# Performance work log

Hardware: AMD Instinct MI355X
Metric: run time of the kernel (lower is better)

## Reference

```python
import jax, jax.numpy as jnp
import numpy as np

LEVELS = 3  # num_basis = 1 + 1 + 2 + 4 = 8


def _haar_basis(x):
    """Closed-form vectorized Haar basis, x: [B, F] raw inputs.

    Replaces the original nested per-feature/per-level/per-bucket mask loops:
    at each level only one bucket k = floor(u*freq) is active, with value
    +2^(level/2) on the left half of the bucket and -2^(level/2) on the right
    half (x == 1.0 falls in the right half of the last bucket, matching the
    torch edge-case handling).
    """
    u = (jnp.tanh(x) + 1.0) / 2.0  # normalize to [0, 1]
    cols = [jnp.ones_like(u)[..., None]]  # scaling function phi
    for level in range(LEVELS):
        freq = 2 ** level
        k = jnp.clip(jnp.floor(u * freq), 0, freq - 1).astype(jnp.int32)  # bucket idx
        mid = (k.astype(u.dtype) + 0.5) / freq
        amp = jnp.asarray(2.0 ** (level / 2), u.dtype)
        sign = jnp.where(u < mid, amp, -amp)  # [B, F]
        cols.append(jax.nn.one_hot(k, freq, dtype=u.dtype) * sign[..., None])
    return jnp.concatenate(cols, axis=-1)  # [B, F, num_basis]


def setup_inputs() -> dict:
    key = jax.random.key(0)
    k1, k2, k3 = jax.random.split(key, 3)
    B, F, O, NB = 32768, 1024, 64, 8
    x = jax.random.normal(k1, (B, F), dtype=jnp.float32)
    coeffs = jax.random.normal(k2, (F, O, NB), dtype=jnp.float32) * 0.05
    base_weight = jax.random.normal(k3, (F, O), dtype=jnp.float32) * 0.05
    return {"x": x, "coeffs": coeffs, "base_weight": base_weight}


def reference(x, coeffs, base_weight):
    basis = _haar_basis(x)                         # [B, F, NB]
    wave_out = jnp.einsum('bin,ion->bo', basis, coeffs)  # [B, O]
    out = wave_out + x @ base_weight               # residual path
    kl = jnp.zeros((1,), dtype=x.dtype)            # non-variational: kl = 0
    return (out, kl)
```

## Files before the change

### kernel.cpp

```cpp
#include <hip/hip_runtime.h>
#include <math.h>


typedef __attribute__((ext_vector_type(8))) short short8;
typedef __attribute__((ext_vector_type(4))) float f32x4;
typedef __attribute__((ext_vector_type(16))) float f32x16;

__device__ __forceinline__ unsigned int f2bf(float f) {
  unsigned int u = __float_as_uint(f);
  u += 0x7FFFu + ((u >> 16) & 1u);
  return u >> 16;
}

__device__ __forceinline__ void gen_basis(int j, unsigned int* d) {
  d[0] = (j < 4) ? 0x3F803F80u : 0xBF803F80u;
  unsigned int sq1 = (j & 2) ? 0xBFB5u : 0x3FB5u;
  d[1] = (j & 4) ? (sq1 << 16) : sq1;
  unsigned long long sd2 = (j & 1) ? 0xC000ull : 0x4000ull;
  unsigned long long d23 = sd2 << ((j & 6) << 3);
  d[2] = (unsigned int)d23;
  d[3] = (unsigned int)(d23 >> 32);
}

#define BARRIER() __asm__ volatile("s_waitcnt lgkmcnt(0)\n\ts_barrier" ::: "memory")

__device__ __forceinline__ void build_run(const float4& xa, const float4& xb,
                                          uint4* __restrict__ dst) {
  float xv[8] = {xa.x, xa.y, xa.z, xa.w, xb.x, xb.y, xb.z, xb.w};
  float t8v[8];
  unsigned int bad = 0;
#pragma unroll
  for (int ff = 0; ff < 8; ++ff) {
    float e = __expf(2.0f * xv[ff]);
    float r = __builtin_amdgcn_rcpf(e + 1.0f);
    float t8 = __builtin_fmaf(-8.0f, r, 8.0f);
    float rn = rintf(t8);
    if (fabsf(t8 - rn) < 3e-5f) bad |= 1u << ff;
    t8v[ff] = t8;
  }
  if (__builtin_expect(bad != 0, 0)) {
#pragma unroll
    for (int ff = 0; ff < 8; ++ff)
      if (bad & (1u << ff)) {
        float tf = (float)tanh((double)xv[ff]);
        t8v[ff] = ((tf + 1.0f) * 0.5f) * 8.0f;
      }
  }
#pragma unroll
  for (int ff = 0; ff < 8; ++ff) {
    int j = (int)t8v[ff]; j = j > 7 ? 7 : j;
    unsigned int d[4];
    gen_basis(j, d);
    uint4 qv; qv.x = d[0]; qv.y = d[1]; qv.z = d[2]; qv.w = d[3];
    dst[ff * 256] = qv;
  }
  uint4 xq;
  xq.x = f2bf(xv[0]) | (f2bf(xv[1]) << 16);
  xq.y = f2bf(xv[2]) | (f2bf(xv[3]) << 16);
  xq.z = f2bf(xv[4]) | (f2bf(xv[5]) << 16);
  xq.w = f2bf(xv[6]) | (f2bf(xv[7]) << 16);
  dst[8 * 256] = xq;
}

__global__ __launch_bounds__(256) void build_w(const float* __restrict__ coeffs,
                                               const float* __restrict__ bw,
                                               uint4* __restrict__ Wsw) {
  const int l = threadIdx.x & 63;
  const int t = threadIdx.x >> 6;
  const int g = blockIdx.x;
  const int c = g / 9, j = g - c * 9;
  const int u = t >> 1, nq = t & 1;
  const int R = c * 4 + 2 * u + (l >> 5);
  const int o = nq * 32 + (l & 31);
  unsigned int dwv[4];
#pragma unroll
  for (int jj = 0; jj < 8; ++jj) {
    int f, n;
    if (j < 8) { f = 8 * R + j;  n = jj; }
    else       { f = 8 * R + jj; n = 8;  }
    float v = (n < 8) ? coeffs[(f * 64 + o) * 8 + n] : bw[f * 64 + o];
    unsigned int hh = f2bf(v);
    if (jj & 1) dwv[jj >> 1] |= hh << 16; else dwv[jj >> 1] = hh;
  }
  uint4 qq; qq.x = dwv[0]; qq.y = dwv[1]; qq.z = dwv[2]; qq.w = dwv[3];
  Wsw[(g * 4 + t) * 64 + l] = qq;
}

#define MFMA32(A, B, C) __builtin_amdgcn_mfma_f32_32x32x16_bf16( \
    __builtin_bit_cast(short8, (A)), __builtin_bit_cast(short8, (B)), (C), 0, 0, 0)

template <int NS>
__device__ __forceinline__ void mfma_main(const uint4* __restrict__ Bsw,
                                          const uint4* __restrict__ Albuf,
                                          f32x16& acc0, f32x16& acc1,
                                          int ks, int nq, int l) {
  const int hi = l >> 5;
  const int l31 = l & 31;
  BARRIER();
  for (int c = 0; c < 32; ++c) {
    const uint4* cur = Albuf + (c & 1) * 2304;
    uint4 Bv[NS][2];
#pragma unroll
    for (int i = 0; i < NS; ++i) {
      const uint4* wp = Bsw + (size_t)(((c * 9 + ks + 2 * i) * 4 + nq) * 64) + l;
      Bv[i][0] = wp[0];
      Bv[i][1] = wp[128];
    }
    __builtin_amdgcn_s_setprio(1);
#pragma unroll
    for (int i = 0; i < NS; ++i) {
      const int s = ks + 2 * i;
      const uint4* rb = cur + s * 256 + hi * 64 + l31;
      uint4 a00 = rb[0];
      uint4 a01 = rb[32];
      uint4 a10 = rb[128];
      uint4 a11 = rb[160];
      acc0 = MFMA32(a00, Bv[i][0], acc0);
      acc0 = MFMA32(a10, Bv[i][1], acc0);
      acc1 = MFMA32(a01, Bv[i][0], acc1);
      acc1 = MFMA32(a11, Bv[i][1], acc1);
    }
    __builtin_amdgcn_s_setprio(0);
    BARRIER();
  }
}

__global__ __launch_bounds__(512, 4) void wavelet_gemm(const float* __restrict__ x,
                                                       const uint4* __restrict__ Bsw,
                                                       float* __restrict__ out,
                                                       int out_size) {
  __shared__ uint4 Albuf[2 * 9 * 256];
  const int tid = threadIdx.x;
  const int l = tid & 63;
  const int w = tid >> 6;
  const long rowbase = (long)blockIdx.x * 64;
  float* P = (float*)Albuf;

  if (w < 4) {
    const int nq = w & 1;
    const int ks = w >> 1;
    f32x16 acc0 = {};
    f32x16 acc1 = {};
    if (ks == 0) mfma_main<5>(Bsw, Albuf, acc0, acc1, 0, nq, l);
    else         mfma_main<4>(Bsw, Albuf, acc0, acc1, 1, nq, l);
    float* Pk = P + ks * 4096;
    const int col   = nq * 32 + (l & 31);
    const int rbase = 4 * (l >> 5);
#pragma unroll
    for (int rg = 0; rg < 16; ++rg) {
      const int grow = (rg & 3) + 8 * (rg >> 2) + rbase;
      Pk[grow * 64 + col]        = acc0[rg];
      Pk[(grow + 32) * 64 + col] = acc1[rg];
    }
    BARRIER();
  } else {
    const int r = w - 4;
    uint4* wr0 = Albuf + r * 64 + l;
    const float* xrow = x + (rowbase + l) * 1024 + r * 8;
    float4 xa = *(const float4*)(xrow);
    float4 xb = *(const float4*)(xrow + 4);
    build_run(xa, xb, wr0);
    xa = *(const float4*)(xrow + 32);
    xb = *(const float4*)(xrow + 36);
    BARRIER();
    for (int c = 0; c < 32; ++c) {
      if (c + 1 < 32) {
        build_run(xa, xb, Albuf + ((c + 1) & 1) * 2304 + r * 64 + l);
        if (c + 2 < 32) {
          xa = *(const float4*)(xrow + (c + 2) * 32);
          xb = *(const float4*)(xrow + (c + 2) * 32 + 4);
        }
      }
      BARRIER();
    }
    BARRIER();
  }

  float* og = out + (size_t)rowbase * 64;
  const int row = tid >> 3;
  const int cb  = (tid & 7) * 8;
  f32x4 v0 = *(const f32x4*)(P + row * 64 + cb);
  f32x4 v1 = *(const f32x4*)(P + row * 64 + cb + 4);
  v0 = v0 + *(const f32x4*)(P + 4096 + row * 64 + cb);
  v1 = v1 + *(const f32x4*)(P + 4096 + row * 64 + cb + 4);
  *(f32x4*)(og + row * 64 + cb)     = v0;
  *(f32x4*)(og + row * 64 + cb + 4) = v1;
  if (blockIdx.x == 0 && tid == 0) out[out_size - 1] = 0.0f;
}

extern "C" void kernel_launch(void* const* d_in, const int* in_sizes, int n_in,
                              void* d_out, int out_size, void* d_ws, size_t ws_size,
                              hipStream_t stream) {
  const float* x      = (const float*)d_in[0];
  const float* coeffs = (const float*)d_in[1];
  const float* bw     = (const float*)d_in[2];
  uint4* Wsw = (uint4*)d_ws;
  float* out = (float*)d_out;

  build_w<<<288, 256, 0, stream>>>(coeffs, bw, Wsw);
  wavelet_gemm<<<512, 512, 0, stream>>>(x, (const uint4*)Wsw, out, out_size);
}
```

Before: 225.3 us.

## Swizzle LDS A-tiles, split waves by M-half, software-pipeline weight loads

The MFMA waves now split work by row half (mh) instead of output-column half, so each wave loads all four weight fragments per K-step and reuses each A fragment for two MFMAs. Weight fragments for the next chunk are prefetched into a 3-deep register ring so global loads overlap the MFMAs. The basis-building waves now coalesce x reads with 4-float quads across 16 rows and write XOR-swizzled LDS addresses to reduce bank conflicts. The epilogue reads partials linearly. The cost is higher register pressure from the B ring, which could hurt occupancy.

After: 234.9 us. 1.04x slower.

```diff
diff --git a/kernel.cpp b/kernel.cpp
--- a/kernel.cpp
+++ b/kernel.cpp
@@ -24,13 +24,13 @@
 
 #define BARRIER() __asm__ volatile("s_waitcnt lgkmcnt(0)\n\ts_barrier" ::: "memory")
 
-__device__ __forceinline__ void build_run(const float4& xa, const float4& xb,
-                                          uint4* __restrict__ dst) {
-  float xv[8] = {xa.x, xa.y, xa.z, xa.w, xb.x, xb.y, xb.z, xb.w};
-  float t8v[8];
+__device__ __forceinline__ void build_half(const float4& xq, uint4* __restrict__ buf,
+                                           int run, int row, int h) {
+  float xv[4] = {xq.x, xq.y, xq.z, xq.w};
+  float t8v[4];
   unsigned int bad = 0;
 #pragma unroll
-  for (int ff = 0; ff < 8; ++ff) {
+  for (int ff = 0; ff < 4; ++ff) {
     float e = __expf(2.0f * xv[ff]);
     float r = __builtin_amdgcn_rcpf(e + 1.0f);
     float t8 = __builtin_fmaf(-8.0f, r, 8.0f);
@@ -40,26 +40,26 @@
   }
   if (__builtin_expect(bad != 0, 0)) {
 #pragma unroll
-    for (int ff = 0; ff < 8; ++ff)
+    for (int ff = 0; ff < 4; ++ff)
       if (bad & (1u << ff)) {
         float tf = (float)tanh((double)xv[ff]);
         t8v[ff] = ((tf + 1.0f) * 0.5f) * 8.0f;
       }
   }
-#pragma unroll
-  for (int ff = 0; ff < 8; ++ff) {
-    int j = (int)t8v[ff]; j = j > 7 ? 7 : j;
+  uint4* dq = buf + run * 64 + (row ^ (2 * run + h));
+#pragma unroll
+  for (int k = 0; k < 4; ++k) {
+    int j = (int)t8v[k]; j = j > 7 ? 7 : j;
     unsigned int d[4];
     gen_basis(j, d);
     uint4 qv; qv.x = d[0]; qv.y = d[1]; qv.z = d[2]; qv.w = d[3];
-    dst[ff * 256] = qv;
-  }
-  uint4 xq;
-  xq.x = f2bf(xv[0]) | (f2bf(xv[1]) << 16);
-  xq.y = f2bf(xv[2]) | (f2bf(xv[3]) << 16);
-  xq.z = f2bf(xv[4]) | (f2bf(xv[5]) << 16);
-  xq.w = f2bf(xv[6]) | (f2bf(xv[7]) << 16);
-  dst[8 * 256] = xq;
+    dq[(4 * h + k) * 256] = qv;
+  }
+  uint2 hv;
+  hv.x = f2bf(xv[0]) | (f2bf(xv[1]) << 16);
+  hv.y = f2bf(xv[2]) | (f2bf(xv[3]) << 16);
+  uint4* dx = buf + 8 * 256 + run * 64 + (row ^ (2 * run + 2));
+  ((uint2*)dx)[h] = hv;
 }
 
 __global__ __launch_bounds__(256) void build_w(const float* __restrict__ coeffs,
@@ -93,34 +93,51 @@
 __device__ __forceinline__ void mfma_main(const uint4* __restrict__ Bsw,
                                           const uint4* __restrict__ Albuf,
                                           f32x16& acc0, f32x16& acc1,
-                                          int ks, int nq, int l) {
+                                          int ks, int mh, int l) {
   const int hi = l >> 5;
   const int l31 = l & 31;
+  int offA[2][3];
+#pragma unroll
+  for (int u = 0; u < 2; ++u)
+#pragma unroll
+    for (int sd = 0; sd < 3; ++sd)
+      offA[u][sd] = (2 * u + hi) * 64 + mh * 32 + (l31 ^ (4 * u + 2 * hi + sd));
+
+  uint4 Bq[3][4];
+#pragma unroll
+  for (int i = 0; i < 3; ++i) {
+    const uint4* wp = Bsw + (size_t)((ks + 2 * i) * 4) * 64 + l;
+    Bq[i][0] = wp[0]; Bq[i][1] = wp[64]; Bq[i][2] = wp[128]; Bq[i][3] = wp[192];
+  }
   BARRIER();
   for (int c = 0; c < 32; ++c) {
     const uint4* cur = Albuf + (c & 1) * 2304;
-    uint4 Bv[NS][2];
-#pragma unroll
-    for (int i = 0; i < NS; ++i) {
-      const uint4* wp = Bsw + (size_t)(((c * 9 + ks + 2 * i) * 4 + nq) * 64) + l;
-      Bv[i][0] = wp[0];
-      Bv[i][1] = wp[128];
-    }
     __builtin_amdgcn_s_setprio(1);
 #pragma unroll
     for (int i = 0; i < NS; ++i) {
       const int s = ks + 2 * i;
-      const uint4* rb = cur + s * 256 + hi * 64 + l31;
-      uint4 a00 = rb[0];
-      uint4 a01 = rb[32];
-      uint4 a10 = rb[128];
-      uint4 a11 = rb[160];
-      acc0 = MFMA32(a00, Bv[i][0], acc0);
-      acc0 = MFMA32(a10, Bv[i][1], acc0);
-      acc1 = MFMA32(a01, Bv[i][0], acc1);
-      acc1 = MFMA32(a11, Bv[i][1], acc1);
+      const int sd = s >> 2;
+      const uint4* rb = cur + s * 256;
+      uint4 a0 = rb[offA[0][sd]];
+      uint4 a1 = rb[offA[1][sd]];
+      acc0 = MFMA32(a0, Bq[i % 3][0], acc0);
+      acc1 = MFMA32(a0, Bq[i % 3][1], acc1);
+      acc0 = MFMA32(a1, Bq[i % 3][2], acc0);
+      acc1 = MFMA32(a1, Bq[i % 3][3], acc1);
+      if (i + 3 < NS) {
+        const uint4* wp = Bsw + (size_t)((c * 9 + ks + 2 * (i + 3)) * 4) * 64 + l;
+        Bq[i % 3][0] = wp[0];   Bq[i % 3][1] = wp[64];
+        Bq[i % 3][2] = wp[128]; Bq[i % 3][3] = wp[192];
+      }
     }
     __builtin_amdgcn_s_setprio(0);
+    if (c + 1 < 32) {
+#pragma unroll
+      for (int i = 0; i < 3; ++i) {
+        const uint4* wp = Bsw + (size_t)(((c + 1) * 9 + ks + 2 * i) * 4) * 64 + l;
+        Bq[i][0] = wp[0]; Bq[i][1] = wp[64]; Bq[i][2] = wp[128]; Bq[i][3] = wp[192];
+      }
+    }
     BARRIER();
   }
 }
@@ -137,38 +154,45 @@
   float* P = (float*)Albuf;
 
   if (w < 4) {
-    const int nq = w & 1;
-    const int ks = w >> 1;
+    const int mh = w >> 1;
+    const int ks = w & 1;
     f32x16 acc0 = {};
     f32x16 acc1 = {};
-    if (ks == 0) mfma_main<5>(Bsw, Albuf, acc0, acc1, 0, nq, l);
-    else         mfma_main<4>(Bsw, Albuf, acc0, acc1, 1, nq, l);
+    if (ks == 0) mfma_main<5>(Bsw, Albuf, acc0, acc1, 0, mh, l);
+    else         mfma_main<4>(Bsw, Albuf, acc0, acc1, 1, mh, l);
     float* Pk = P + ks * 4096;
-    const int col   = nq * 32 + (l & 31);
-    const int rbase = 4 * (l >> 5);
+    const int colb = l & 31;
+    const int rb32 = mh * 32 + 4 * (l >> 5);
 #pragma unroll
     for (int rg = 0; rg < 16; ++rg) {
-      const int grow = (rg & 3) + 8 * (rg >> 2) + rbase;
-      Pk[grow * 64 + col]        = acc0[rg];
-      Pk[(grow + 32) * 64 + col] = acc1[rg];
+      const int grow = (rg & 3) + 8 * (rg >> 2) + rb32;
+      Pk[grow * 64 + colb]      = acc0[rg];
+      Pk[grow * 64 + 32 + colb] = acc1[rg];
     }
     BARRIER();
   } else {
-    const int r = w - 4;
-    uint4* wr0 = Albuf + r * 64 + l;
-    const float* xrow = x + (rowbase + l) * 1024 + r * 8;
-    float4 xa = *(const float4*)(xrow);
-    float4 xb = *(const float4*)(xrow + 4);
-    build_run(xa, xb, wr0);
-    xa = *(const float4*)(xrow + 32);
-    xb = *(const float4*)(xrow + 36);
+    const int b = w - 4;
+    const int quad = l & 7;
+    const int run = quad >> 1, h = quad & 1;
+    const int row0 = 16 * b + (l >> 3);
+    const int row1 = row0 + 8;
+    const float* xp0 = x + (rowbase + row0) * 1024 + quad * 4;
+    const float* xp1 = x + (rowbase + row1) * 1024 + quad * 4;
+    float4 xa0 = *(const float4*)(xp0);
+    float4 xa1 = *(const float4*)(xp1);
+    build_half(xa0, Albuf, run, row0, h);
+    build_half(xa1, Albuf, run, row1, h);
+    xa0 = *(const float4*)(xp0 + 32);
+    xa1 = *(const float4*)(xp1 + 32);
     BARRIER();
     for (int c = 0; c < 32; ++c) {
       if (c + 1 < 32) {
-        build_run(xa, xb, Albuf + ((c + 1) & 1) * 2304 + r * 64 + l);
+        uint4* nb = Albuf + ((c + 1) & 1) * 2304;
+        build_half(xa0, nb, run, row0, h);
+        build_half(xa1, nb, run, row1, h);
         if (c + 2 < 32) {
-          xa = *(const float4*)(xrow + (c + 2) * 32);
-          xb = *(const float4*)(xrow + (c + 2) * 32 + 4);
+          xa0 = *(const float4*)(xp0 + (c + 2) * 32);
+          xa1 = *(const float4*)(xp1 + (c + 2) * 32);
         }
       }
       BARRIER();
@@ -177,14 +201,11 @@
   }
 
   float* og = out + (size_t)rowbase * 64;
-  const int row = tid >> 3;
-  const int cb  = (tid & 7) * 8;
-  f32x4 v0 = *(const f32x4*)(P + row * 64 + cb);
-  f32x4 v1 = *(const f32x4*)(P + row * 64 + cb + 4);
-  v0 = v0 + *(const f32x4*)(P + 4096 + row * 64 + cb);
-  v1 = v1 + *(const f32x4*)(P + 4096 + row * 64 + cb + 4);
-  *(f32x4*)(og + row * 64 + cb)     = v0;
-  *(f32x4*)(og + row * 64 + cb + 4) = v1;
+  const int d = tid * 4;
+  f32x4 v0 = *(const f32x4*)(P + d)        + *(const f32x4*)(P + 4096 + d);
+  f32x4 v1 = *(const f32x4*)(P + 2048 + d) + *(const f32x4*)(P + 6144 + d);
+  *(f32x4*)(og + d) = v0;
+  *(f32x4*)(og + 2048 + d) = v1;
   if (blockIdx.x == 0 && tid == 0) out[out_size - 1] = 0.0f;
 }
 
```

## Build basis fragments in registers per wave, drop LDS producer/consumer pipeline

Applied to the files above, without the earlier changes.

Replaces the producer/consumer split, where four waves build Haar basis tiles into double-buffered LDS and four waves run MFMA, with a scheme where all eight waves build their own A fragments directly in registers and feed MFMA. Work is split by K-slice and by M-half, and the four partial accumulators are reduced through LDS at the end. This removes the per-chunk barriers and LDS traffic of the A tiles. In exchange, each wave recomputes tanh for its own lanes and issues more global loads of x and weights.

Result: slower. 271.9 us (+20.7%).

```diff
diff --git a/kernel.cpp b/kernel.cpp
--- a/kernel.cpp
+++ b/kernel.cpp
@@ -20,46 +20,6 @@
   unsigned long long d23 = sd2 << ((j & 6) << 3);
   d[2] = (unsigned int)d23;
   d[3] = (unsigned int)(d23 >> 32);
-}
-
-#define BARRIER() __asm__ volatile("s_waitcnt lgkmcnt(0)\n\ts_barrier" ::: "memory")
-
-__device__ __forceinline__ void build_run(const float4& xa, const float4& xb,
-                                          uint4* __restrict__ dst) {
-  float xv[8] = {xa.x, xa.y, xa.z, xa.w, xb.x, xb.y, xb.z, xb.w};
-  float t8v[8];
-  unsigned int bad = 0;
-#pragma unroll
-  for (int ff = 0; ff < 8; ++ff) {
-    float e = __expf(2.0f * xv[ff]);
-    float r = __builtin_amdgcn_rcpf(e + 1.0f);
-    float t8 = __builtin_fmaf(-8.0f, r, 8.0f);
-    float rn = rintf(t8);
-    if (fabsf(t8 - rn) < 3e-5f) bad |= 1u << ff;
-    t8v[ff] = t8;
-  }
-  if (__builtin_expect(bad != 0, 0)) {
-#pragma unroll
-    for (int ff = 0; ff < 8; ++ff)
-      if (bad & (1u << ff)) {
-        float tf = (float)tanh((double)xv[ff]);
-        t8v[ff] = ((tf + 1.0f) * 0.5f) * 8.0f;
-      }
-  }
-#pragma unroll
-  for (int ff = 0; ff < 8; ++ff) {
-    int j = (int)t8v[ff]; j = j > 7 ? 7 : j;
-    unsigned int d[4];
-    gen_basis(j, d);
-    uint4 qv; qv.x = d[0]; qv.y = d[1]; qv.z = d[2]; qv.w = d[3];
-    dst[ff * 256] = qv;
-  }
-  uint4 xq;
-  xq.x = f2bf(xv[0]) | (f2bf(xv[1]) << 16);
-  xq.y = f2bf(xv[2]) | (f2bf(xv[3]) << 16);
-  xq.z = f2bf(xv[4]) | (f2bf(xv[5]) << 16);
-  xq.w = f2bf(xv[6]) | (f2bf(xv[7]) << 16);
-  dst[8 * 256] = xq;
 }
 
 __global__ __launch_bounds__(256) void build_w(const float* __restrict__ coeffs,
@@ -89,102 +49,106 @@
 #define MFMA32(A, B, C) __builtin_amdgcn_mfma_f32_32x32x16_bf16( \
     __builtin_bit_cast(short8, (A)), __builtin_bit_cast(short8, (B)), (C), 0, 0, 0)
 
-template <int NS>
-__device__ __forceinline__ void mfma_main(const uint4* __restrict__ Bsw,
-                                          const uint4* __restrict__ Albuf,
-                                          f32x16& acc0, f32x16& acc1,
-                                          int ks, int nq, int l) {
-  const int hi = l >> 5;
-  const int l31 = l & 31;
-  BARRIER();
-  for (int c = 0; c < 32; ++c) {
-    const uint4* cur = Albuf + (c & 1) * 2304;
-    uint4 Bv[NS][2];
-#pragma unroll
-    for (int i = 0; i < NS; ++i) {
-      const uint4* wp = Bsw + (size_t)(((c * 9 + ks + 2 * i) * 4 + nq) * 64) + l;
-      Bv[i][0] = wp[0];
-      Bv[i][1] = wp[128];
-    }
-    __builtin_amdgcn_s_setprio(1);
-#pragma unroll
-    for (int i = 0; i < NS; ++i) {
-      const int s = ks + 2 * i;
-      const uint4* rb = cur + s * 256 + hi * 64 + l31;
-      uint4 a00 = rb[0];
-      uint4 a01 = rb[32];
-      uint4 a10 = rb[128];
-      uint4 a11 = rb[160];
-      acc0 = MFMA32(a00, Bv[i][0], acc0);
-      acc0 = MFMA32(a10, Bv[i][1], acc0);
-      acc1 = MFMA32(a01, Bv[i][0], acc1);
-      acc1 = MFMA32(a11, Bv[i][1], acc1);
-    }
-    __builtin_amdgcn_s_setprio(0);
-    BARRIER();
-  }
-}
-
 __global__ __launch_bounds__(512, 4) void wavelet_gemm(const float* __restrict__ x,
                                                        const uint4* __restrict__ Bsw,
                                                        float* __restrict__ out,
                                                        int out_size) {
-  __shared__ uint4 Albuf[2 * 9 * 256];
+  __shared__ float P[4 * 4096];
   const int tid = threadIdx.x;
   const int l = tid & 63;
   const int w = tid >> 6;
+  const int ks = w >> 1;
+  const int mh = w & 1;
+  const int hi = l >> 5;
+  const int l31 = l & 31;
   const long rowbase = (long)blockIdx.x * 64;
-  float* P = (float*)Albuf;
+  const float* xr = x + (rowbase + mh * 32 + l31) * 1024;
+  const int sA = 2 * ks;
+  const int xduty = (ks < 2);
+  const int xrun = 2 * ks + hi;
 
-  if (w < 4) {
-    const int nq = w & 1;
-    const int ks = w >> 1;
-    f32x16 acc0 = {};
-    f32x16 acc1 = {};
-    if (ks == 0) mfma_main<5>(Bsw, Albuf, acc0, acc1, 0, nq, l);
-    else         mfma_main<4>(Bsw, Albuf, acc0, acc1, 1, nq, l);
-    float* Pk = P + ks * 4096;
-    const int col   = nq * 32 + (l & 31);
-    const int rbase = 4 * (l >> 5);
+  f32x16 acc0 = {};
+  f32x16 acc1 = {};
+
+#pragma unroll 1
+  for (int c = 0; c < 32; ++c) {
+    const int cb = 32 * c;
+    const uint4* wp = Bsw + ((size_t)(c * 9 + sA) * 4) * 64 + l;
+    uint4 BA0 = wp[0],   BA1 = wp[64],  BA2 = wp[128], BA3 = wp[192];
+    uint4 BB0 = wp[256], BB1 = wp[320], BB2 = wp[384], BB3 = wp[448];
+    float2 f20 = *(const float2*)(xr + cb + 8 * hi + sA);
+    float2 f21 = *(const float2*)(xr + cb + 8 * (2 + hi) + sA);
+
+    float xv[4] = {f20.x, f20.y, f21.x, f21.y};
+    float t8v[4];
+    unsigned int bad = 0;
 #pragma unroll
-    for (int rg = 0; rg < 16; ++rg) {
-      const int grow = (rg & 3) + 8 * (rg >> 2) + rbase;
-      Pk[grow * 64 + col]        = acc0[rg];
-      Pk[(grow + 32) * 64 + col] = acc1[rg];
+    for (int ff = 0; ff < 4; ++ff) {
+      float e = __expf(2.0f * xv[ff]);
+      float r = __builtin_amdgcn_rcpf(e + 1.0f);
+      float t8 = __builtin_fmaf(-8.0f, r, 8.0f);
+      float rn = rintf(t8);
+      if (fabsf(t8 - rn) < 3e-5f) bad |= 1u << ff;
+      t8v[ff] = t8;
     }
-    BARRIER();
-  } else {
-    const int r = w - 4;
-    uint4* wr0 = Albuf + r * 64 + l;
-    const float* xrow = x + (rowbase + l) * 1024 + r * 8;
-    float4 xa = *(const float4*)(xrow);
-    float4 xb = *(const float4*)(xrow + 4);
-    build_run(xa, xb, wr0);
-    xa = *(const float4*)(xrow + 32);
-    xb = *(const float4*)(xrow + 36);
-    BARRIER();
-    for (int c = 0; c < 32; ++c) {
-      if (c + 1 < 32) {
-        build_run(xa, xb, Albuf + ((c + 1) & 1) * 2304 + r * 64 + l);
-        if (c + 2 < 32) {
-          xa = *(const float4*)(xrow + (c + 2) * 32);
-          xb = *(const float4*)(xrow + (c + 2) * 32 + 4);
+    if (__builtin_expect(bad != 0, 0)) {
+#pragma unroll
+      for (int ff = 0; ff < 4; ++ff)
+        if (bad & (1u << ff)) {
+          float tf = (float)tanh((double)xv[ff]);
+          t8v[ff] = ((tf + 1.0f) * 0.5f) * 8.0f;
         }
-      }
-      BARRIER();
     }
-    BARRIER();
+    uint4 A[4];
+#pragma unroll
+    for (int ff = 0; ff < 4; ++ff) {
+      int j = (int)t8v[ff]; j = j > 7 ? 7 : j;
+      unsigned int d[4];
+      gen_basis(j, d);
+      A[ff].x = d[0]; A[ff].y = d[1]; A[ff].z = d[2]; A[ff].w = d[3];
+    }
+    acc0 = MFMA32(A[0], BA0, acc0);
+    acc1 = MFMA32(A[0], BA1, acc1);
+    acc0 = MFMA32(A[2], BA2, acc0);
+    acc1 = MFMA32(A[2], BA3, acc1);
+    acc0 = MFMA32(A[1], BB0, acc0);
+    acc1 = MFMA32(A[1], BB1, acc1);
+    acc0 = MFMA32(A[3], BB2, acc0);
+    acc1 = MFMA32(A[3], BB3, acc1);
+    if (xduty) {
+      const uint4* wx = Bsw + ((size_t)(c * 9 + 8) * 4) * 64 + l;
+      uint4 BXa = wx[(2 * ks) * 64];
+      uint4 BXb = wx[(2 * ks + 1) * 64];
+      float4 xo0 = *(const float4*)(xr + cb + 8 * xrun);
+      float4 xo1 = *(const float4*)(xr + cb + 8 * xrun + 4);
+      uint4 xa;
+      xa.x = f2bf(xo0.x) | (f2bf(xo0.y) << 16);
+      xa.y = f2bf(xo0.z) | (f2bf(xo0.w) << 16);
+      xa.z = f2bf(xo1.x) | (f2bf(xo1.y) << 16);
+      xa.w = f2bf(xo1.z) | (f2bf(xo1.w) << 16);
+      acc0 = MFMA32(xa, BXa, acc0);
+      acc1 = MFMA32(xa, BXb, acc1);
+    }
   }
 
+  float* Pk = P + ks * 4096;
+  const int rbase = 32 * mh + 4 * hi;
+#pragma unroll
+  for (int rg = 0; rg < 16; ++rg) {
+    const int grow = (rg & 3) + 8 * (rg >> 2) + rbase;
+    Pk[grow * 64 + l31]      = acc0[rg];
+    Pk[grow * 64 + 32 + l31] = acc1[rg];
+  }
+  __syncthreads();
+
   float* og = out + (size_t)rowbase * 64;
-  const int row = tid >> 3;
-  const int cb  = (tid & 7) * 8;
-  f32x4 v0 = *(const f32x4*)(P + row * 64 + cb);
-  f32x4 v1 = *(const f32x4*)(P + row * 64 + cb + 4);
-  v0 = v0 + *(const f32x4*)(P + 4096 + row * 64 + cb);
-  v1 = v1 + *(const f32x4*)(P + 4096 + row * 64 + cb + 4);
-  *(f32x4*)(og + row * 64 + cb)     = v0;
-  *(f32x4*)(og + row * 64 + cb + 4) = v1;
+  const int d = tid * 4;
+  f32x4 v0 = *(const f32x4*)(P + d) + *(const f32x4*)(P + 4096 + d)
+           + *(const f32x4*)(P + 8192 + d) + *(const f32x4*)(P + 12288 + d);
+  f32x4 v1 = *(const f32x4*)(P + 2048 + d) + *(const f32x4*)(P + 6144 + d)
+           + *(const f32x4*)(P + 10240 + d) + *(const f32x4*)(P + 14336 + d);
+  *(f32x4*)(og + d) = v0;
+  *(f32x4*)(og + 2048 + d) = v1;
   if (blockIdx.x == 0 && tid == 0) out[out_size - 1] = 0.0f;
 }
 
```
